# Kernel optimization log

Hardware: AMD Instinct MI355X
Metric: run time of the kernel (lower is better)

## Reference

```python
import jax, jax.numpy as jnp
import numpy as np

B, S, H = 2, 2048, 4096
NQ, NKV, D = 32, 8, 128
EPS = 1e-6
THETA = 1000000.0


def rms_norm(x, w, eps=EPS):
    # normalize over last dim (per-head RMSNorm on head_dim)
    var = jnp.mean(jnp.square(x), axis=-1, keepdims=True)
    return x * jax.lax.rsqrt(var + eps) * w


def rope(x, positions, theta=THETA):
    # x: [B, S, N, D]; rotate-half convention (Qwen/Llama style)
    d = x.shape[-1]
    inv_freq = 1.0 / (theta ** (jnp.arange(0, d, 2, dtype=jnp.float32) / d))  # [D/2]
    ang = positions[:, None].astype(jnp.float32) * inv_freq[None, :]          # [S, D/2]
    cos = jnp.cos(ang)[None, :, None, :]
    sin = jnp.sin(ang)[None, :, None, :]
    x1, x2 = x[..., : d // 2], x[..., d // 2 :]
    return jnp.concatenate([x1 * cos - x2 * sin, x2 * cos + x1 * sin], axis=-1)


def setup_inputs() -> dict:
    key = jax.random.key(0)
    ks = jax.random.split(key, 7)
    sc_in = 1.0 / np.sqrt(H)
    sc_out = 1.0 / np.sqrt(NQ * D)
    return {
        "x": jax.random.normal(ks[0], (B, S, H), jnp.float32),
        "wq": jax.random.normal(ks[1], (H, NQ * D), jnp.float32) * sc_in,
        "wk": jax.random.normal(ks[2], (H, NKV * D), jnp.float32) * sc_in,
        "wv": jax.random.normal(ks[3], (H, NKV * D), jnp.float32) * sc_in,
        "wo": jax.random.normal(ks[4], (NQ * D, H), jnp.float32) * sc_out,
        "q_norm_w": jnp.ones((D,), jnp.float32),
        "k_norm_w": jnp.ones((D,), jnp.float32),
    }


def reference(x, wq, wk, wv, wo, q_norm_w, k_norm_w):
    b, s, _ = x.shape
    positions = jnp.arange(s)

    q = (x @ wq).reshape(b, s, NQ, D)   # [B,S,NQ,D]
    k = (x @ wk).reshape(b, s, NKV, D)  # [B,S,NKV,D]
    v = (x @ wv).reshape(b, s, NKV, D)

    # per-head QK RMSNorm, then RoPE
    q = rope(rms_norm(q, q_norm_w), positions)
    k = rope(rms_norm(k, k_norm_w), positions)

    # GQA: expand kv heads to query heads (group = NQ // NKV)
    g = NQ // NKV
    k = jnp.repeat(k, g, axis=2)  # [B,S,NQ,D]
    v = jnp.repeat(v, g, axis=2)

    scale = D ** -0.5
    scores = jnp.einsum("bqhd,bkhd->bhqk", q, k) * scale  # [B,NQ,S,S]
    causal = jnp.tril(jnp.ones((s, s), bool))
    scores = jnp.where(causal[None, None], scores, jnp.finfo(scores.dtype).min)
    attn = jax.nn.softmax(scores, axis=-1)

    out = jnp.einsum("bhqk,bkhd->bqhd", attn, v).reshape(b, s, NQ * D)
    return out @ wo
```

## Files before the change

kernel.cpp:

```cpp
#include <hip/hip_runtime.h>
#include <hip/hip_bf16.h>

#define DEV __device__ __forceinline__

typedef unsigned short u16;
typedef unsigned int u32;
typedef __attribute__((ext_vector_type(8))) short short8;
typedef __attribute__((ext_vector_type(4))) float f32x4;
typedef __attribute__((ext_vector_type(16))) float f32x16;

static constexpr int Bb = 2, Ss = 2048, Hh = 4096, NQ = 32, NKV = 8, Dd = 128;
static constexpr int Mm = Bb * Ss;

DEV u16 f2bf(float f) {
    u32 u = __float_as_uint(f);
    u32 r = (u + 0x7fffu + ((u >> 16) & 1u)) >> 16;
    return (u16)r;
}
DEV float bf2f(u16 b) { return __uint_as_float((u32)b << 16); }
DEV u32 cvtpk(float lo, float hi) {
    u32 r;
    asm("v_cvt_pk_bf16_f32 %0, %1, %2" : "=v"(r) : "v"(lo), "v"(hi));
    return r;
}

__global__ void k_cast(const float4* __restrict__ in, ushort4* __restrict__ out, int n4) {
    int i = blockIdx.x * 256 + threadIdx.x;
    if (i < n4) {
        float4 v = in[i];
        ushort4 o;
        o.x = f2bf(v.x); o.y = f2bf(v.y); o.z = f2bf(v.z); o.w = f2bf(v.w);
        out[i] = o;
    }
}

__global__ void k_transpose(const float* __restrict__ in, u16* __restrict__ out, int R, int C) {
    __shared__ float t[32][33];
    int lx = threadIdx.x & 31, ly = threadIdx.x >> 5;
    long tc = (long)blockIdx.x * 32, tr = (long)blockIdx.y * 32;
    #pragma unroll
    for (int i = 0; i < 32; i += 8) t[ly + i][lx] = in[(tr + ly + i) * C + tc + lx];
    __syncthreads();
    #pragma unroll
    for (int i = 0; i < 32; i += 8) out[(tc + ly + i) * R + tr + lx] = f2bf(t[lx][ly + i]);
}

DEV void gld16(const void* g, void* l) {
    __builtin_amdgcn_global_load_lds((const __attribute__((address_space(1))) void*)g,
                                     (__attribute__((address_space(3))) void*)l, 16, 0, 0);
}

#define FENCE asm volatile("" ::: "memory")

template <int MODE>
__global__ __launch_bounds__(512) void k_gemm256(const u16* __restrict__ A, const u16* __restrict__ B0,
                                                 void* __restrict__ C0, void* __restrict__ C1,
                                                 void* __restrict__ C2, int M, int N, int K, int nbx) {
    constexpr int NF = (MODE == 3) ? 3 : 4;
    constexpr int LPT = 4 + NF;
    __shared__ u16 S[2][16384 + NF * 4096];
    const int tid = threadIdx.x, lane = tid & 63, wid = tid >> 6;
    const int wr = wid >> 2, wc = wid & 3;
    const int l = blockIdx.x;
    const int bx = l % nbx, by = l / nbx;
    const long m0 = (long)by * 256, n0 = (long)bx * (NF * 64);
    const int r15 = lane & 15;
    const int cch0 = 8 * ((lane >> 4) ^ (r15 & 7));

    const u16 *pA[4], *pB[NF];
    {
        int rl = lane >> 3;
        int sc = 8 * ((lane & 7) ^ rl);
        #pragma unroll
        for (int j = 0; j < 4; j++)
            pA[j] = A + (m0 + (wid * 4 + j) * 8 + rl) * (long)K + sc;
        #pragma unroll
        for (int j = 0; j < NF; j++)
            pB[j] = B0 + (n0 + (wid * NF + j) * 8 + rl) * (long)K + sc;
    }

    f32x4 acc[8][NF];
    #pragma unroll
    for (int i = 0; i < 8; i++)
        #pragma unroll
        for (int j = 0; j < NF; j++) acc[i][j] = f32x4{0.f, 0.f, 0.f, 0.f};

    const int NT = K / 64;
    auto STAGE_A = [&](int t) {
        int tb = t & 1; long ko = (long)t * 64;
        #pragma unroll
        for (int j = 0; j < 4; j++) gld16(pA[j] + ko, (void*)&S[tb][(wid * 4 + j) * 512]);
    };
    auto STAGE_B = [&](int t) {
        int tb = t & 1; long ko = (long)t * 64;
        #pragma unroll
        for (int j = 0; j < NF; j++) gld16(pB[j] + ko, (void*)&S[tb][16384 + (wid * NF + j) * 512]);
    };

    const int aro = wr * 8192 + r15 * 64 + cch0;
    const int bro = 16384 + wc * (NF * 1024) + r15 * 64 + cch0;

    STAGE_B(0); STAGE_A(0); STAGE_B(1); STAGE_A(1);
    asm volatile("s_waitcnt vmcnt(%0)" ::"i"(LPT) : "memory");
    FENCE; __builtin_amdgcn_s_barrier(); FENCE;

    short8 af[4][2], bf[NF][2];
    for (int kt = 0; kt < NT; ++kt) {
        const u16* Sb = S[kt & 1];
        #pragma unroll
        for (int n = 0; n < NF; n++) {
            bf[n][0] = *(const short8*)&Sb[bro + n * 1024];
            bf[n][1] = *(const short8*)&Sb[(bro + n * 1024) ^ 32];
        }
        #pragma unroll
        for (int m = 0; m < 4; m++) {
            af[m][0] = *(const short8*)&Sb[aro + m * 1024];
            af[m][1] = *(const short8*)&Sb[(aro + m * 1024) ^ 32];
        }
        __builtin_amdgcn_s_setprio(1);
        #pragma unroll
        for (int m = 0; m < 4; m++)
            #pragma unroll
            for (int n = 0; n < NF; n++) {
                acc[m][n] = __builtin_amdgcn_mfma_f32_16x16x32_bf16(af[m][0], bf[n][0], acc[m][n], 0, 0, 0);
                acc[m][n] = __builtin_amdgcn_mfma_f32_16x16x32_bf16(af[m][1], bf[n][1], acc[m][n], 0, 0, 0);
            }
        __builtin_amdgcn_s_setprio(0);
        short8 ag[4][2];
        #pragma unroll
        for (int m = 0; m < 4; m++) {
            ag[m][0] = *(const short8*)&Sb[aro + (m + 4) * 1024];
            ag[m][1] = *(const short8*)&Sb[(aro + (m + 4) * 1024) ^ 32];
        }
        FENCE; __builtin_amdgcn_s_barrier(); FENCE;
        if (kt + 2 < NT) STAGE_B(kt + 2);
        __builtin_amdgcn_s_setprio(1);
        #pragma unroll
        for (int m = 0; m < 4; m++)
            #pragma unroll
            for (int n = 0; n < NF; n++) {
                acc[m + 4][n] = __builtin_amdgcn_mfma_f32_16x16x32_bf16(ag[m][0], bf[n][0], acc[m + 4][n], 0, 0, 0);
                acc[m + 4][n] = __builtin_amdgcn_mfma_f32_16x16x32_bf16(ag[m][1], bf[n][1], acc[m + 4][n], 0, 0, 0);
            }
        __builtin_amdgcn_s_setprio(0);
        FENCE; __builtin_amdgcn_s_barrier(); FENCE;
        if (kt + 2 < NT) {
            STAGE_A(kt + 2);
            asm volatile("s_waitcnt vmcnt(%0)" ::"i"(LPT) : "memory");
        } else {
            asm volatile("s_waitcnt vmcnt(0)" ::: "memory");
        }
        FENCE; __builtin_amdgcn_s_barrier(); FENCE;
    }

    const int rq = (lane >> 4) * 4;
    #pragma unroll
    for (int m = 0; m < 8; m++) {
        #pragma unroll
        for (int n = 0; n < NF; n++) {
            long row0 = m0 + wr * 128 + m * 16 + rq;
            long col = n0 + wc * (NF * 16) + n * 16 + r15;
            if (MODE == 0) {
                float* Cf = (float*)C0;
                #pragma unroll
                for (int i = 0; i < 4; i++) Cf[(row0 + i) * N + col] = acc[m][n][i];
            } else {
                if (col < 4096) {
                    u16* Cb = (u16*)C0;
                    #pragma unroll
                    for (int i = 0; i < 4; i++) Cb[(row0 + i) * 4096 + col] = f2bf(acc[m][n][i]);
                } else if (col < 5120) {
                    u16* Cb = (u16*)C1;
                    long cl = col - 4096;
                    #pragma unroll
                    for (int i = 0; i < 4; i++) Cb[(row0 + i) * 1024 + cl] = f2bf(acc[m][n][i]);
                } else {
                    u16* Cb = (u16*)C2;
                    long cl = col - 5120;
                    ushort4 pk;
                    pk.x = f2bf(acc[m][n][0]);
                    pk.y = f2bf(acc[m][n][1]);
                    pk.z = f2bf(acc[m][n][2]);
                    pk.w = f2bf(acc[m][n][3]);
                    *(ushort4*)&Cb[cl * Mm + row0] = pk;
                }
            }
        }
    }
}

__global__ __launch_bounds__(256) void k_normrope(u16* __restrict__ buf,
                                                  const float* __restrict__ w, int NH, float oscale) {
    int row = blockIdx.x * 4 + (threadIdx.x >> 6);
    int lane = threadIdx.x & 63;
    long base = (long)row * 128;
    float x1 = bf2f(buf[base + lane]), x2 = bf2f(buf[base + lane + 64]);
    float ss = x1 * x1 + x2 * x2;
    #pragma unroll
    for (int m = 1; m < 64; m <<= 1) ss += __shfl_xor(ss, m);
    float r = rsqrtf(ss * (1.f / 128.f) + 1e-6f);
    float n1 = x1 * r * w[lane], n2 = x2 * r * w[lane + 64];
    int pos = (row / NH) % Ss;
    float invf = exp2f((float)lane * (-19.931568569324174f / 64.f));
    float ang = (float)pos * invf;
    float c = cosf(ang), sn = sinf(ang);
    buf[base + lane] = f2bf((n1 * c - n2 * sn) * oscale);
    buf[base + lane + 64] = f2bf((n2 * c + n1 * sn) * oscale);
}

__global__ __launch_bounds__(256, 2) void k_attn(const u16* __restrict__ Q, const u16* __restrict__ Kb,
                                                 const u16* __restrict__ Vg, u16* __restrict__ O) {
    __shared__ u16 KT[2][64 * 128];
    __shared__ u16 VT[2][128 * 64];
    int tid = threadIdx.x, lane = tid & 63, wid = tid >> 6;
    int d0 = blockIdx.x;
    int L = (d0 & 7) * 64 + (d0 >> 3);
    int pr = L & 31;
    int hk = (L >> 5) & 7;
    int b = L >> 8;
    int h = hk * 4 + wid;
    int q0a = pr * 32;
    int q0b = (63 - pr) * 32;
    int c31 = lane & 31, hi5 = lane >> 5;
    int kx16 = (c31 & 15) << 3;
    int kx8 = (c31 & 7) << 3;

    short8 qfa[8], qfb[8];
    {
        const u16* qra = Q + ((long)(b * Ss + q0a + c31) * NQ + h) * Dd + hi5 * 8;
        const u16* qrb = Q + ((long)(b * Ss + q0b + c31) * NQ + h) * Dd + hi5 * 8;
        #pragma unroll
        for (int c = 0; c < 8; c++) {
            qfa[c] = *(const short8*)(qra + c * 16);
            qfb[c] = *(const short8*)(qrb + c * 16);
        }
    }

    const u16* kg[4];
    const u16* vg[4];
    int i0 = wid * 4;
    #pragma unroll
    for (int ii = 0; ii < 4; ii++) {
        int i = i0 + ii;
        int r = i * 4 + (lane >> 4);
        kg[ii] = Kb + ((long)(b * Ss + r) * NKV + hk) * Dd + 8 * ((lane & 15) ^ (r & 15));
        int d = i * 8 + (lane >> 3);
        vg[ii] = Vg + (long)(hk * Dd + d) * Mm + (long)b * Ss + 8 * ((lane & 7) ^ (d & 7));
    }

    f32x16 oaa[4], oab[4];
    #pragma unroll
    for (int f = 0; f < 4; f++)
        #pragma unroll
        for (int r = 0; r < 16; r++) { oaa[f][r] = 0.f; oab[f][r] = 0.f; }
    float mra = -INFINITY, lra = 0.f, mrb = -INFINITY, lrb = 0.f;

    const long kadv = (long)64 * NKV * Dd;
    int nt = q0b / 64 + 1;
    int cur = 0;

    auto STEP = [&](int k0, int q0, const short8 (&qf)[8], f32x16 (&oa)[4],
                    float& mrun, float& lrun) {
        int ql = q0 + c31;
        int krow = k0 & 32;
        f32x16 st;
        #pragma unroll
        for (int r = 0; r < 16; r++) st[r] = 0.f;
        __builtin_amdgcn_s_setprio(1);
        #pragma unroll
        for (int c = 0; c < 8; c++) {
            short8 kf = *(const short8*)&KT[cur][(krow + c31) * 128 + ((c * 16 + hi5 * 8) ^ kx16)];
            st = __builtin_amdgcn_mfma_f32_32x32x16_bf16(kf, qf[c], st, 0, 0, 0);
        }
        __builtin_amdgcn_s_setprio(0);
        float p[16];
        if (k0 + 31 > q0) {
            #pragma unroll
            for (int r = 0; r < 16; r++) {
                int kidx = k0 + (r & 3) + 8 * (r >> 2) + 4 * hi5;
                p[r] = (kidx > ql) ? -INFINITY : st[r];
            }
        } else {
            #pragma unroll
            for (int r = 0; r < 16; r++) p[r] = st[r];
        }
        float pmax = p[0];
        #pragma unroll
        for (int r = 1; r < 16; r++) pmax = fmaxf(pmax, p[r]);
        pmax = fmaxf(pmax, __shfl_xor(pmax, 32));
        if (!__all(pmax - mrun <= 8.f)) {
            float mnew = fmaxf(mrun, pmax);
            float sc = __builtin_amdgcn_exp2f(mrun - mnew);
            lrun *= sc;
            #pragma unroll
            for (int f = 0; f < 4; f++)
                #pragma unroll
                for (int r = 0; r < 16; r++) oa[f][r] *= sc;
            mrun = mnew;
        }
        float ls = 0.f;
        #pragma unroll
        for (int r = 0; r < 16; r++) {
            float e = __builtin_amdgcn_exp2f(p[r] - mrun);
            p[r] = e;
            ls += e;
        }
        ls += __shfl_xor(ls, 32);
        lrun += ls;

        u32 w0 = cvtpk(p[0], p[1]), w1 = cvtpk(p[2], p[3]);
        u32 w2 = cvtpk(p[4], p[5]), w3 = cvtpk(p[6], p[7]);
        u32 w4 = cvtpk(p[8], p[9]), w5 = cvtpk(p[10], p[11]);
        u32 w6 = cvtpk(p[12], p[13]), w7 = cvtpk(p[14], p[15]);
        u32 x0 = (u32)__shfl_xor((int)w0, 32), x1 = (u32)__shfl_xor((int)w1, 32);
        u32 x2 = (u32)__shfl_xor((int)w2, 32), x3 = (u32)__shfl_xor((int)w3, 32);
        u32 x4 = (u32)__shfl_xor((int)w4, 32), x5 = (u32)__shfl_xor((int)w5, 32);
        u32 x6 = (u32)__shfl_xor((int)w6, 32), x7 = (u32)__shfl_xor((int)w7, 32);
        union { u32 u[4]; short8 s; } pb0, pb1;
        if (hi5) {
            pb0.u[0] = x2; pb0.u[1] = x3; pb0.u[2] = w2; pb0.u[3] = w3;
            pb1.u[0] = x6; pb1.u[1] = x7; pb1.u[2] = w6; pb1.u[3] = w7;
        } else {
            pb0.u[0] = w0; pb0.u[1] = w1; pb0.u[2] = x0; pb0.u[3] = x1;
            pb1.u[0] = w4; pb1.u[1] = w5; pb1.u[2] = x4; pb1.u[3] = x5;
        }
        __builtin_amdgcn_s_setprio(1);
        #pragma unroll
        for (int f = 0; f < 4; f++) {
            int d = 32 * f + c31;
            const u16* vrow = &VT[cur][d * 64];
            short8 v0 = *(const short8*)&vrow[(krow + hi5 * 8) ^ kx8];
            short8 v1 = *(const short8*)&vrow[(krow + 16 + hi5 * 8) ^ kx8];
            oa[f] = __builtin_amdgcn_mfma_f32_32x32x16_bf16(v0, pb0.s, oa[f], 0, 0, 0);
            oa[f] = __builtin_amdgcn_mfma_f32_32x32x16_bf16(v1, pb1.s, oa[f], 0, 0, 0);
        }
        __builtin_amdgcn_s_setprio(0);
    };

    #pragma unroll
    for (int ii = 0; ii < 4; ii++) {
        gld16(kg[ii], &KT[0][(i0 + ii) * 512]);
        gld16(vg[ii], &VT[0][(i0 + ii) * 512]);
    }
    __syncthreads();

    for (int t = 0; t < nt; ++t) {
        if (t + 1 < nt) {
            long ko = (long)(t + 1) * kadv;
            int vo = (t + 1) * 64;
            #pragma unroll
            for (int ii = 0; ii < 4; ii++) {
                gld16(kg[ii] + ko, &KT[cur ^ 1][(i0 + ii) * 512]);
                gld16(vg[ii] + vo, &VT[cur ^ 1][(i0 + ii) * 512]);
            }
        }
        #pragma unroll
        for (int ks = 0; ks < 2; ++ks) {
            int k0 = t * 64 + ks * 32;
            if (k0 <= q0a + 31) STEP(k0, q0a, qfa, oaa, mra, lra);
            if (k0 <= q0b + 31) STEP(k0, q0b, qfb, oab, mrb, lrb);
        }
        __syncthreads();
        cur ^= 1;
    }

    #pragma unroll
    for (int x = 0; x < 2; x++) {
        int q0 = x ? q0b : q0a;
        f32x16* oa = x ? oab : oaa;
        float linv = 1.f / (x ? lrb : lra);
        u16* orow = O + ((long)(b * Ss + q0 + c31) * NQ + h) * Dd;
        #pragma unroll
        for (int f = 0; f < 4; f++) {
            #pragma unroll
            for (int rq = 0; rq < 4; rq++) {
                int dbase = 32 * f + 8 * rq + 4 * hi5;
                union { u32 u[2]; ushort4 v; } pk;
                pk.u[0] = cvtpk(oa[f][4 * rq + 0] * linv, oa[f][4 * rq + 1] * linv);
                pk.u[1] = cvtpk(oa[f][4 * rq + 2] * linv, oa[f][4 * rq + 3] * linv);
                *(ushort4*)(orow + dbase) = pk.v;
            }
        }
    }
}

extern "C" void kernel_launch(void* const* d_in, const int* in_sizes, int n_in,
                              void* d_out, int out_size, void* d_ws, size_t ws_size,
                              hipStream_t stream) {
    (void)in_sizes; (void)n_in; (void)out_size; (void)ws_size;
    const float* x = (const float*)d_in[0];
    const float* wq = (const float*)d_in[1];
    const float* wk = (const float*)d_in[2];
    const float* wv = (const float*)d_in[3];
    const float* wo = (const float*)d_in[4];
    const float* qnw = (const float*)d_in[5];
    const float* knw = (const float*)d_in[6];

    char* ws = (char*)d_ws;
    const size_t MB = 1024 * 1024;
    const float qscale = (float)(0.08838834764831845 * 1.4426950408889634);

    u16* xb = (u16*)(ws);
    u16* Wqkv = (u16*)(ws + 32 * MB);
    u16* qb = (u16*)(ws + 80 * MB);
    u16* kb = (u16*)(ws + 112 * MB);
    u16* vt = (u16*)(ws + 120 * MB);
    u16* ao = xb;
    u16* WoT = Wqkv;

    int n4 = Mm * Hh / 4;
    k_cast<<<n4 / 256, 256, 0, stream>>>((const float4*)x, (ushort4*)xb, n4);

    k_transpose<<<dim3(Hh / 32, Hh / 32), 256, 0, stream>>>(wq, Wqkv, Hh, Hh);
    k_transpose<<<dim3((NKV * Dd) / 32, Hh / 32), 256, 0, stream>>>(wk, Wqkv + (size_t)4096 * Hh, Hh, NKV * Dd);
    k_transpose<<<dim3((NKV * Dd) / 32, Hh / 32), 256, 0, stream>>>(wv, Wqkv + (size_t)5120 * Hh, Hh, NKV * Dd);

    k_gemm256<3><<<32 * (Mm / 256), 512, 0, stream>>>(xb, Wqkv, qb, kb, vt, Mm, 6144, Hh, 32);

    k_normrope<<<(Mm * NQ) / 4, 256, 0, stream>>>(qb, qnw, NQ, qscale);
    k_normrope<<<(Mm * NKV) / 4, 256, 0, stream>>>(kb, knw, NKV, 1.0f);

    k_attn<<<512, 256, 0, stream>>>(qb, kb, vt, ao);

    k_transpose<<<dim3(Hh / 32, Hh / 32), 256, 0, stream>>>(wo, WoT, Hh, Hh);
    k_gemm256<0><<<16 * (Mm / 256), 512, 0, stream>>>(ao, WoT, d_out, nullptr, nullptr, Mm, Hh, NQ * Dd, 16);
}
```

Measured before the change: 535.3 us.

## Drop double-buffered GEMM pipeline for single-buffer with higher occupancy and smaller output tiles

Replaces the two-stage LDS double buffer and its hand-placed vmcnt waits and barriers in the GEMM with a single LDS buffer that is loaded and synchronized with __syncthreads each k-step. It also adds a minimum of 4 blocks per multiprocessor to the launch bounds and narrows the output-projection tile (NF from 4 to 2), which doubles its grid. The aim is to get more resident blocks by using less LDS and fewer registers, and to hide memory latency that way instead of through software prefetch. The cost is that loads no longer overlap with MFMA inside a block and there are more barriers per iteration.

```diff
diff --git a/kernel.cpp b/kernel.cpp
--- a/kernel.cpp
+++ b/kernel.cpp
@@ -50,15 +50,12 @@
                                      (__attribute__((address_space(3))) void*)l, 16, 0, 0);
 }
 
-#define FENCE asm volatile("" ::: "memory")
-
 template <int MODE>
-__global__ __launch_bounds__(512) void k_gemm256(const u16* __restrict__ A, const u16* __restrict__ B0,
-                                                 void* __restrict__ C0, void* __restrict__ C1,
-                                                 void* __restrict__ C2, int M, int N, int K, int nbx) {
-    constexpr int NF = (MODE == 3) ? 3 : 4;
-    constexpr int LPT = 4 + NF;
-    __shared__ u16 S[2][16384 + NF * 4096];
+__global__ __launch_bounds__(512, 4) void k_gemm256(const u16* __restrict__ A, const u16* __restrict__ B0,
+                                                    void* __restrict__ C0, void* __restrict__ C1,
+                                                    void* __restrict__ C2, int M, int N, int K, int nbx) {
+    constexpr int NF = (MODE == 3) ? 3 : 2;
+    __shared__ u16 S[16384 + NF * 4096];
     const int tid = threadIdx.x, lane = tid & 63, wid = tid >> 6;
     const int wr = wid >> 2, wc = wid & 3;
     const int l = blockIdx.x;
@@ -86,36 +83,26 @@
         for (int j = 0; j < NF; j++) acc[i][j] = f32x4{0.f, 0.f, 0.f, 0.f};
 
     const int NT = K / 64;
-    auto STAGE_A = [&](int t) {
-        int tb = t & 1; long ko = (long)t * 64;
-        #pragma unroll
-        for (int j = 0; j < 4; j++) gld16(pA[j] + ko, (void*)&S[tb][(wid * 4 + j) * 512]);
-    };
-    auto STAGE_B = [&](int t) {
-        int tb = t & 1; long ko = (long)t * 64;
-        #pragma unroll
-        for (int j = 0; j < NF; j++) gld16(pB[j] + ko, (void*)&S[tb][16384 + (wid * NF + j) * 512]);
-    };
-
     const int aro = wr * 8192 + r15 * 64 + cch0;
     const int bro = 16384 + wc * (NF * 1024) + r15 * 64 + cch0;
 
-    STAGE_B(0); STAGE_A(0); STAGE_B(1); STAGE_A(1);
-    asm volatile("s_waitcnt vmcnt(%0)" ::"i"(LPT) : "memory");
-    FENCE; __builtin_amdgcn_s_barrier(); FENCE;
-
     short8 af[4][2], bf[NF][2];
     for (int kt = 0; kt < NT; ++kt) {
-        const u16* Sb = S[kt & 1];
+        long ko = (long)kt * 64;
+        #pragma unroll
+        for (int j = 0; j < 4; j++) gld16(pA[j] + ko, (void*)&S[(wid * 4 + j) * 512]);
+        #pragma unroll
+        for (int j = 0; j < NF; j++) gld16(pB[j] + ko, (void*)&S[16384 + (wid * NF + j) * 512]);
+        __syncthreads();
         #pragma unroll
         for (int n = 0; n < NF; n++) {
-            bf[n][0] = *(const short8*)&Sb[bro + n * 1024];
-            bf[n][1] = *(const short8*)&Sb[(bro + n * 1024) ^ 32];
+            bf[n][0] = *(const short8*)&S[bro + n * 1024];
+            bf[n][1] = *(const short8*)&S[(bro + n * 1024) ^ 32];
         }
         #pragma unroll
         for (int m = 0; m < 4; m++) {
-            af[m][0] = *(const short8*)&Sb[aro + m * 1024];
-            af[m][1] = *(const short8*)&Sb[(aro + m * 1024) ^ 32];
+            af[m][0] = *(const short8*)&S[aro + m * 1024];
+            af[m][1] = *(const short8*)&S[(aro + m * 1024) ^ 32];
         }
         __builtin_amdgcn_s_setprio(1);
         #pragma unroll
@@ -129,11 +116,9 @@
         short8 ag[4][2];
         #pragma unroll
         for (int m = 0; m < 4; m++) {
-            ag[m][0] = *(const short8*)&Sb[aro + (m + 4) * 1024];
-            ag[m][1] = *(const short8*)&Sb[(aro + (m + 4) * 1024) ^ 32];
-        }
-        FENCE; __builtin_amdgcn_s_barrier(); FENCE;
-        if (kt + 2 < NT) STAGE_B(kt + 2);
+            ag[m][0] = *(const short8*)&S[aro + (m + 4) * 1024];
+            ag[m][1] = *(const short8*)&S[(aro + (m + 4) * 1024) ^ 32];
+        }
         __builtin_amdgcn_s_setprio(1);
         #pragma unroll
         for (int m = 0; m < 4; m++)
@@ -143,14 +128,7 @@
                 acc[m + 4][n] = __builtin_amdgcn_mfma_f32_16x16x32_bf16(ag[m][1], bf[n][1], acc[m + 4][n], 0, 0, 0);
             }
         __builtin_amdgcn_s_setprio(0);
-        FENCE; __builtin_amdgcn_s_barrier(); FENCE;
-        if (kt + 2 < NT) {
-            STAGE_A(kt + 2);
-            asm volatile("s_waitcnt vmcnt(%0)" ::"i"(LPT) : "memory");
-        } else {
-            asm volatile("s_waitcnt vmcnt(0)" ::: "memory");
-        }
-        FENCE; __builtin_amdgcn_s_barrier(); FENCE;
+        __syncthreads();
     }
 
     const int rq = (lane >> 4) * 4;
@@ -423,5 +401,5 @@
     k_attn<<<512, 256, 0, stream>>>(qb, kb, vt, ao);
 
     k_transpose<<<dim3(Hh / 32, Hh / 32), 256, 0, stream>>>(wo, WoT, Hh, Hh);
-    k_gemm256<0><<<16 * (Mm / 256), 512, 0, stream>>>(ao, WoT, d_out, nullptr, nullptr, Mm, Hh, NQ * Dd, 16);
-}
+    k_gemm256<0><<<32 * (Mm / 256), 512, 0, stream>>>(ao, WoT, d_out, nullptr, nullptr, Mm, Hh, NQ * Dd, 32);
+}
```

New measurement: 1.515 ms. +183.1%, slower.
